# Performance work log

Measured on AMD Instinct MI355X. Metric: run time of the kernel, lower is better.

The kernel has to match this reference:

```python
import jax, jax.numpy as jnp
import numpy as np

N, F, T, B, E, G = 50000, 3, 32, 32, 100000, 64
R = 1.1

def setup_inputs() -> dict:
    key = jax.random.key(0)
    k1, k2, k3, k4 = jax.random.split(key, 4)
    x = jax.random.normal(k1, (N, F), dtype=jnp.float32)
    v = jax.random.uniform(k2, (F, T), dtype=jnp.float32) - 0.5  # torch.rand(...) - 0.5
    lin = jnp.linspace(-R, R, B, dtype=jnp.float32).reshape(B, 1, 1)
    edge_index = jax.random.randint(k3, (2, E), 0, N)
    batch = jnp.sort(jax.random.randint(k4, (N,), 0, G))  # sorted graph ids per node
    return {"x": x, "v": v, "lin": lin, "edge_index": edge_index,
            "batch": batch, "num_graphs": G}


def _compute_ecc(h, index, lin, dim_size):
    # h: (M, T) heights; lin: (B,1,1); broadcast sigmoid -> (B, M, T)
    ecc = jax.nn.sigmoid(200.0 * (lin - h))
    # segment-sum over the M axis per graph; torch's segment_coo(...).movedim(0,1)
    # yields (dim_size, B, T), which equals segment_sum over axis 0 of (M, B, T).
    return jax.ops.segment_sum(jnp.moveaxis(ecc, 1, 0), index, num_segments=dim_size)


def reference(x, v, lin, edge_index, batch, num_graphs):
    nh = x @ v                                   # (N, T) node heights
    eh = jnp.max(nh[edge_index], axis=0)         # (E, T) edge max-gather
    ect_nodes = _compute_ecc(nh, batch, lin, num_graphs)                     # (G, B, T)
    ect_edges = _compute_ecc(eh, batch[edge_index[0]], lin, num_graphs)      # (G, B, T)
    return ect_nodes - ect_edges
```

## Files before the change

### kernel.cpp

```cpp
#include <hip/hip_runtime.h>

#define WG 256
#define G64 64
#define SPLITS 16

__global__ __launch_bounds__(WG) void k_bucket(const int* __restrict__ edge,
                                               const int* __restrict__ batch,
                                               const float* __restrict__ x,
                                               float4* __restrict__ bucket,
                                               int* __restrict__ cursor,
                                               int* __restrict__ node_off,
                                               int E, int N, int CAP) {
    __shared__ int lc[G64], lb[G64];
    int tid = threadIdx.x;
    if (tid < G64) lc[tid] = 0;
    __syncthreads();
    int e = blockIdx.x * WG + tid;
    int g = 0, r = 0, s = 0, d = 0;
    if (e < E) {
        s = edge[e];
        d = edge[E + e];
        g = batch[s];
        r = atomicAdd(&lc[g], 1);
    }
    __syncthreads();
    if (tid < G64 && lc[tid]) lb[tid] = atomicAdd(&cursor[tid], lc[tid]);
    __syncthreads();
    if (e < E) {
        int pos = lb[g] + r;
        if (pos < CAP) {
            const float* xs = x + (size_t)s * 3;
            const float* xd = x + (size_t)d * 3;
            size_t o = ((size_t)g * CAP + pos) * 2;
            bucket[o]     = make_float4(xs[0], xs[1], xs[2], 0.f);
            bucket[o + 1] = make_float4(xd[0], xd[1], xd[2], 0.f);
        }
    }
    if (blockIdx.x == 0 && tid <= G64) {
        int lo = 0, hi = N;
        while (lo < hi) {
            int mid = (lo + hi) >> 1;
            if (batch[mid] < tid) lo = mid + 1; else hi = mid;
        }
        node_off[tid] = lo;
    }
}

__global__ __launch_bounds__(WG) void k_acc(const float* __restrict__ x,
                                            const float* __restrict__ v,
                                            const float4* __restrict__ bucket,
                                            const float* __restrict__ lin,
                                            const int* __restrict__ cursor,
                                            const int* __restrict__ node_off,
                                            float* __restrict__ out, int CAP) {
    int g = blockIdx.x;
    int n0 = node_off[g], n1 = node_off[g + 1];
    int nn = n1 - n0;
    int ne = cursor[g]; if (ne > CAP) ne = CAP;
    int L = nn + ne;
    int ipc = (L + SPLITS - 1) / SPLITS;
    int lo = blockIdx.y * ipc;
    int hi = lo + ipc; if (hi > L) hi = L;

    int tid = threadIdx.x, t = tid & 31, sub = tid >> 5;
    float v0 = v[t], v1 = v[32 + t], v2 = v[64 + t];

    float lin0 = lin[0];
    float dlin = lin[1] - lin[0];
    const float LOG2E = 1.4426950408889634f;
    float D2 = 200.f * dlin * LOG2E;
    float inv_dlin = 1.f / dlin;
    float fstep = exp2f(-D2);

    float acc[32];
#pragma unroll
    for (int b = 0; b < 32; ++b) acc[b] = 0.f;

    int nhi = hi < nn ? hi : nn;
    for (int idx = lo + sub; idx < nhi; idx += 8) {
        const float* xr = x + (size_t)(n0 + idx) * 3;
        float h = xr[0] * v0 + xr[1] * v1 + xr[2] * v2;
        float bs = (h - lin0) * inv_dlin;
        float bF = floorf(bs);
        float e0 = exp2f((bs - bF) * D2);
        float s0 = __builtin_amdgcn_rcpf(1.f + e0);
        float s1 = __builtin_amdgcn_rcpf(fmaf(e0, fstep, 1.f));
        float m = s1 - s0;
        float base = fmaf(-bF, m, s0);
#pragma unroll
        for (int b = 0; b < 32; ++b)
            acc[b] += __builtin_amdgcn_fmed3f(fmaf(m, (float)b, base), 0.f, 1.f);
    }

    int elo = lo > nn ? lo : nn;
    for (int idx = elo + sub; idx < hi; idx += 8) {
        size_t o = ((size_t)g * CAP + (idx - nn)) * 2;
        float4 a = bucket[o];
        float4 c = bucket[o + 1];
        float hs = a.x * v0 + a.y * v1 + a.z * v2;
        float hd = c.x * v0 + c.y * v1 + c.z * v2;
        float h = fmaxf(hs, hd);
        float bs = (h - lin0) * inv_dlin;
        float bF = floorf(bs);
        float e0 = exp2f((bs - bF) * D2);
        float s0 = __builtin_amdgcn_rcpf(1.f + e0);
        float s1 = __builtin_amdgcn_rcpf(fmaf(e0, fstep, 1.f));
        float m = -(s1 - s0);
        float base = fmaf(bF, -m, -s0) * -1.f;
        base = fmaf(-bF, m, -s0);
#pragma unroll
        for (int b = 0; b < 32; ++b)
            acc[b] += __builtin_amdgcn_fmed3f(fmaf(m, (float)b, base), -1.f, 0.f);
    }

    __shared__ float stage[4 * 1024];
#pragma unroll
    for (int b = 0; b < 32; ++b) acc[b] += __shfl_xor(acc[b], 32, 64);
    int w = tid >> 6;
    if ((tid & 32) == 0) {
#pragma unroll
        for (int b = 0; b < 32; ++b) stage[(w << 10) + (b << 5) + t] = acc[b];
    }
    __syncthreads();
    for (int c = tid; c < 1024; c += WG) {
        float s = stage[c] + stage[1024 + c] + stage[2048 + c] + stage[3072 + c];
        unsafeAtomicAdd(&out[(g << 10) + c], s);
    }
}

extern "C" void kernel_launch(void* const* d_in, const int* in_sizes, int n_in,
                              void* d_out, int out_size, void* d_ws, size_t ws_size,
                              hipStream_t stream) {
    const float* x     = (const float*)d_in[0];
    const float* v     = (const float*)d_in[1];
    const float* lin   = (const float*)d_in[2];
    const int*   edge  = (const int*)d_in[3];
    const int*   batch = (const int*)d_in[4];
    int N = in_sizes[4];
    int E = in_sizes[3] / 2;

    float* out = (float*)d_out;

    int* cursor   = (int*)d_ws;
    int* node_off = cursor + G64;
    float4* bucket = (float4*)((char*)d_ws + 1024);
    long long cap_ws = (long long)((ws_size - 1024) / ((size_t)G64 * 32));
    int CAP = (int)(cap_ws < (long long)E ? cap_ws : (long long)E);

    hipMemsetAsync(out, 0, (size_t)out_size * sizeof(float), stream);
    hipMemsetAsync(cursor, 0, G64 * sizeof(int), stream);

    k_bucket<<<(E + WG - 1) / WG, WG, 0, stream>>>(edge, batch, x, bucket,
                                                   cursor, node_off, E, N, CAP);
    dim3 grid(G64, SPLITS);
    k_acc<<<grid, WG, 0, stream>>>(x, v, bucket, lin, cursor, node_off, out, CAP);
}
```

Before: 98.37 us.

## Replace per-bin sigmoid sums with difference histogram and prefix scan

Each element now adds three sigmoid deltas into a shared-memory difference histogram via LDS atomics instead of evaluating 32 clamped linear terms per bin. A per-column prefix sum rebuilds the cumulative values before the global atomic flush. The bucket pass now stores only int2 edge indices, so the accumulate kernel gathers x itself. The output memset is folded into the bucket kernel. This cuts per-element ALU work and bucket traffic, but adds LDS atomic contention and random gathers of x in the accumulate kernel.

```diff
diff --git a/kernel.cpp b/kernel.cpp
--- a/kernel.cpp
+++ b/kernel.cpp
@@ -6,16 +6,23 @@
 
 __global__ __launch_bounds__(WG) void k_bucket(const int* __restrict__ edge,
                                                const int* __restrict__ batch,
-                                               const float* __restrict__ x,
-                                               float4* __restrict__ bucket,
+                                               int2* __restrict__ bucket,
                                                int* __restrict__ cursor,
                                                int* __restrict__ node_off,
+                                               float* __restrict__ out,
                                                int E, int N, int CAP) {
     __shared__ int lc[G64], lb[G64];
     int tid = threadIdx.x;
+    int bid = blockIdx.x;
     if (tid < G64) lc[tid] = 0;
+
+    if (bid < G64) {
+        float4* o4 = (float4*)(out + ((size_t)bid << 10));
+        o4[tid] = make_float4(0.f, 0.f, 0.f, 0.f);
+    }
     __syncthreads();
-    int e = blockIdx.x * WG + tid;
+
+    int e = bid * WG + tid;
     int g = 0, r = 0, s = 0, d = 0;
     if (e < E) {
         s = edge[e];
@@ -28,15 +35,10 @@
     __syncthreads();
     if (e < E) {
         int pos = lb[g] + r;
-        if (pos < CAP) {
-            const float* xs = x + (size_t)s * 3;
-            const float* xd = x + (size_t)d * 3;
-            size_t o = ((size_t)g * CAP + pos) * 2;
-            bucket[o]     = make_float4(xs[0], xs[1], xs[2], 0.f);
-            bucket[o + 1] = make_float4(xd[0], xd[1], xd[2], 0.f);
-        }
+        if (pos < CAP) bucket[(size_t)g * CAP + pos] = make_int2(s, d);
     }
-    if (blockIdx.x == 0 && tid <= G64) {
+
+    if (bid == 0 && tid <= G64) {
         int lo = 0, hi = N;
         while (lo < hi) {
             int mid = (lo + hi) >> 1;
@@ -48,11 +50,15 @@
 
 __global__ __launch_bounds__(WG) void k_acc(const float* __restrict__ x,
                                             const float* __restrict__ v,
-                                            const float4* __restrict__ bucket,
+                                            const int2* __restrict__ bucket,
                                             const float* __restrict__ lin,
                                             const int* __restrict__ cursor,
                                             const int* __restrict__ node_off,
                                             float* __restrict__ out, int CAP) {
+    __shared__ float hist[34 * 32];
+    int tid = threadIdx.x;
+    for (int i = tid; i < 34 * 32; i += WG) hist[i] = 0.f;
+
     int g = blockIdx.x;
     int n0 = node_off[g], n1 = node_off[g + 1];
     int nn = n1 - n0;
@@ -62,19 +68,16 @@
     int lo = blockIdx.y * ipc;
     int hi = lo + ipc; if (hi > L) hi = L;
 
-    int tid = threadIdx.x, t = tid & 31, sub = tid >> 5;
+    int t = tid & 31, sub = tid >> 5;
     float v0 = v[t], v1 = v[32 + t], v2 = v[64 + t];
 
     float lin0 = lin[0];
     float dlin = lin[1] - lin[0];
     const float LOG2E = 1.4426950408889634f;
-    float D2 = 200.f * dlin * LOG2E;
+    float d2 = 200.f * dlin * LOG2E;
     float inv_dlin = 1.f / dlin;
-    float fstep = exp2f(-D2);
-
-    float acc[32];
-#pragma unroll
-    for (int b = 0; b < 32; ++b) acc[b] = 0.f;
+    float fstep = exp2f(-d2);
+    __syncthreads();
 
     int nhi = hi < nn ? hi : nn;
     for (int idx = lo + sub; idx < nhi; idx += 8) {
@@ -82,60 +85,62 @@
         float h = xr[0] * v0 + xr[1] * v1 + xr[2] * v2;
         float bs = (h - lin0) * inv_dlin;
         float bF = floorf(bs);
-        float e0 = exp2f((bs - bF) * D2);
+        float e0 = exp2f((bs - bF) * d2);
         float s0 = __builtin_amdgcn_rcpf(1.f + e0);
         float s1 = __builtin_amdgcn_rcpf(fmaf(e0, fstep, 1.f));
-        float m = s1 - s0;
-        float base = fmaf(-bF, m, s0);
-#pragma unroll
-        for (int b = 0; b < 32; ++b)
-            acc[b] += __builtin_amdgcn_fmed3f(fmaf(m, (float)b, base), 0.f, 1.f);
+        int ib = (int)bF;
+        int i0 = min(33, max(0, ib));
+        int i1 = min(33, max(0, ib + 1));
+        int i2 = min(33, max(0, ib + 2));
+        atomicAdd(&hist[i0 * 32 + t], s0);
+        atomicAdd(&hist[i1 * 32 + t], s1 - s0);
+        atomicAdd(&hist[i2 * 32 + t], 1.f - s1);
     }
 
     int elo = lo > nn ? lo : nn;
     for (int idx = elo + sub; idx < hi; idx += 8) {
-        size_t o = ((size_t)g * CAP + (idx - nn)) * 2;
-        float4 a = bucket[o];
-        float4 c = bucket[o + 1];
-        float hs = a.x * v0 + a.y * v1 + a.z * v2;
-        float hd = c.x * v0 + c.y * v1 + c.z * v2;
+        int2 sd = bucket[(size_t)g * CAP + (idx - nn)];
+        const float* xs = x + (size_t)sd.x * 3;
+        const float* xd = x + (size_t)sd.y * 3;
+        float hs = xs[0] * v0 + xs[1] * v1 + xs[2] * v2;
+        float hd = xd[0] * v0 + xd[1] * v1 + xd[2] * v2;
         float h = fmaxf(hs, hd);
         float bs = (h - lin0) * inv_dlin;
         float bF = floorf(bs);
-        float e0 = exp2f((bs - bF) * D2);
+        float e0 = exp2f((bs - bF) * d2);
         float s0 = __builtin_amdgcn_rcpf(1.f + e0);
         float s1 = __builtin_amdgcn_rcpf(fmaf(e0, fstep, 1.f));
-        float m = -(s1 - s0);
-        float base = fmaf(bF, -m, -s0) * -1.f;
-        base = fmaf(-bF, m, -s0);
-#pragma unroll
-        for (int b = 0; b < 32; ++b)
-            acc[b] += __builtin_amdgcn_fmed3f(fmaf(m, (float)b, base), -1.f, 0.f);
+        int ib = (int)bF;
+        int i0 = min(33, max(0, ib));
+        int i1 = min(33, max(0, ib + 1));
+        int i2 = min(33, max(0, ib + 2));
+        atomicAdd(&hist[i0 * 32 + t], -s0);
+        atomicAdd(&hist[i1 * 32 + t], s0 - s1);
+        atomicAdd(&hist[i2 * 32 + t], s1 - 1.f);
     }
 
-    __shared__ float stage[4 * 1024];
+    __syncthreads();
+    if (tid < 32) {
+        float run = 0.f;
 #pragma unroll
-    for (int b = 0; b < 32; ++b) acc[b] += __shfl_xor(acc[b], 32, 64);
-    int w = tid >> 6;
-    if ((tid & 32) == 0) {
-#pragma unroll
-        for (int b = 0; b < 32; ++b) stage[(w << 10) + (b << 5) + t] = acc[b];
+        for (int b = 0; b < 32; ++b) {
+            run += hist[b * 32 + tid];
+            hist[b * 32 + tid] = run;
+        }
     }
     __syncthreads();
-    for (int c = tid; c < 1024; c += WG) {
-        float s = stage[c] + stage[1024 + c] + stage[2048 + c] + stage[3072 + c];
-        unsafeAtomicAdd(&out[(g << 10) + c], s);
-    }
+    for (int c = tid; c < 1024; c += WG)
+        unsafeAtomicAdd(&out[((size_t)g << 10) + c], hist[c]);
 }
 
 extern "C" void kernel_launch(void* const* d_in, const int* in_sizes, int n_in,
                               void* d_out, int out_size, void* d_ws, size_t ws_size,
                               hipStream_t stream) {
+    const int*   edge  = (const int*)d_in[3];
+    const int*   batch = (const int*)d_in[4];
     const float* x     = (const float*)d_in[0];
     const float* v     = (const float*)d_in[1];
     const float* lin   = (const float*)d_in[2];
-    const int*   edge  = (const int*)d_in[3];
-    const int*   batch = (const int*)d_in[4];
     int N = in_sizes[4];
     int E = in_sizes[3] / 2;
 
@@ -143,15 +148,14 @@
 
     int* cursor   = (int*)d_ws;
     int* node_off = cursor + G64;
-    float4* bucket = (float4*)((char*)d_ws + 1024);
-    long long cap_ws = (long long)((ws_size - 1024) / ((size_t)G64 * 32));
+    int2* bucket  = (int2*)((char*)d_ws + 1024);
+    long long cap_ws = (long long)((ws_size - 1024) / ((size_t)G64 * sizeof(int2)));
     int CAP = (int)(cap_ws < (long long)E ? cap_ws : (long long)E);
 
-    hipMemsetAsync(out, 0, (size_t)out_size * sizeof(float), stream);
     hipMemsetAsync(cursor, 0, G64 * sizeof(int), stream);
 
-    k_bucket<<<(E + WG - 1) / WG, WG, 0, stream>>>(edge, batch, x, bucket,
-                                                   cursor, node_off, E, N, CAP);
+    k_bucket<<<(E + WG - 1) / WG, WG, 0, stream>>>(edge, batch, bucket, cursor,
+                                                   node_off, out, E, N, CAP);
     dim3 grid(G64, SPLITS);
     k_acc<<<grid, WG, 0, stream>>>(x, v, bucket, lin, cursor, node_off, out, CAP);
 }
```

New measurement: 155.6 us. +58.1%, slower.
